# Optimization experiments

Hardware: AMD Instinct MI355X
Metric: run time of the kernel (lower is better)

The kernel has to match this reference:

```python
import jax, jax.numpy as jnp
import numpy as np

EMA_W = 0.99


def setup_inputs() -> dict:
    key = jax.random.key(0)
    k1, k2 = jax.random.split(key)
    B, C, H, W = 16, 8, 512, 512
    generated_masks = jax.random.normal(k1, (B, C, H, W), dtype=jnp.float32)
    prev_dist = jax.random.uniform(k2, (C,), dtype=jnp.float32)
    prev_dist = prev_dist / jnp.sum(prev_dist)  # a valid running distribution
    return {"generated_masks": generated_masks, "prev_dist": prev_dist}


def reference(generated_masks, prev_dist):
    # generated_masks: [B, C, H, W]; prev_dist: [C]
    B, C, H, W = generated_masks.shape
    num_classes = C
    norm_factor = 1.0 / num_classes

    # per-pixel argmax over channels -> [B, H, W]
    mask_classes = jnp.argmax(generated_masks, axis=1)

    # histogram over classes (fused equivalent of torch.unique + scatter)
    hist = jnp.zeros((num_classes,), dtype=jnp.float32).at[
        mask_classes.reshape(-1)
    ].add(1.0)

    total = B * H * W
    class_distribution = prev_dist * EMA_W + (1.0 - EMA_W) * hist / total

    balance = jnp.linalg.norm(
        (class_distribution - norm_factor) / (1.0 - norm_factor)
    )
    return balance, class_distribution
```

## Files before the change

kernel.cpp:

```cpp
#include <hip/hip_runtime.h>
#include <math.h>

#define HW        262144
#define HWQ       65536
#define CHW       2097152
#define NGROUPS   1048576
#define NBLOCKS   2048
#define NTHREADS  256
#define GSTRIDE   524288
#define TOTAL_PX  4194304.0f

__global__ __launch_bounds__(NTHREADS, 8)
void argmax_hist_kernel(const float* __restrict__ masks,
                        unsigned int* __restrict__ partial) {
    const int tid = threadIdx.x;
    int cnt[8] = {0, 0, 0, 0, 0, 0, 0, 0};

    const int gbase = blockIdx.x * NTHREADS + tid;

    #pragma unroll
    for (int it = 0; it < 2; ++it) {
        const int g   = gbase + it * GSTRIDE;
        const int b   = g >> 16;
        const int hw4 = (g & 65535) << 2;
        const float4* p = (const float4*)(masks + (size_t)b * CHW + hw4);

        float4 v0 = p[0];
        float4 v1 = p[1 * HWQ];
        float4 v2 = p[2 * HWQ];
        float4 v3 = p[3 * HWQ];
        float4 v4 = p[4 * HWQ];
        float4 v5 = p[5 * HWQ];
        float4 v6 = p[6 * HWQ];
        float4 v7 = p[7 * HWQ];

        float bv0 = v0.x, bv1 = v0.y, bv2 = v0.z, bv3 = v0.w;
        int   bi0 = 0,    bi1 = 0,    bi2 = 0,    bi3 = 0;

        #define STEP(vv, c)                                                   \
            bi0 = ((vv).x > bv0) ? (c) : bi0;  bv0 = ((vv).x > bv0) ? (vv).x : bv0; \
            bi1 = ((vv).y > bv1) ? (c) : bi1;  bv1 = ((vv).y > bv1) ? (vv).y : bv1; \
            bi2 = ((vv).z > bv2) ? (c) : bi2;  bv2 = ((vv).z > bv2) ? (vv).z : bv2; \
            bi3 = ((vv).w > bv3) ? (c) : bi3;  bv3 = ((vv).w > bv3) ? (vv).w : bv3;
        STEP(v1, 1) STEP(v2, 2) STEP(v3, 3) STEP(v4, 4)
        STEP(v5, 5) STEP(v6, 6) STEP(v7, 7)
        #undef STEP

        #pragma unroll
        for (int k = 0; k < 8; ++k) {
            cnt[k] += (bi0 == k) + (bi1 == k) + (bi2 == k) + (bi3 == k);
        }
    }

    #pragma unroll
    for (int k = 0; k < 8; ++k) {
        #pragma unroll
        for (int off = 32; off >= 1; off >>= 1) {
            cnt[k] += __shfl_down(cnt[k], off, 64);
        }
    }

    __shared__ int lds[32];
    const int lane = tid & 63;
    const int wid  = tid >> 6;
    if (lane == 0) {
        #pragma unroll
        for (int k = 0; k < 8; ++k) lds[wid * 8 + k] = cnt[k];
    }
    __syncthreads();
    if (tid < 8) {
        unsigned int s = (unsigned int)(lds[tid] + lds[8 + tid] + lds[16 + tid] + lds[24 + tid]);
        partial[blockIdx.x * 8 + tid] = s;
    }
}

__global__ __launch_bounds__(256)
void finalize_kernel(const unsigned int* __restrict__ partial,
                     const float* __restrict__ prev,
                     float* __restrict__ out) {
    __shared__ float s[256];
    const int t = threadIdx.x;
    const int c = t & 7;
    const int j = t >> 3;

    unsigned int sum = 0;
    for (int row = j; row < NBLOCKS; row += 32) {
        sum += partial[row * 8 + c];
    }
    s[t] = (float)sum;
    __syncthreads();

    if (t < 8) {
        float h = 0.0f;
        #pragma unroll
        for (int k = 0; k < 32; ++k) h += s[t + 8 * k];
        float dist = prev[t] * 0.99f + 0.01f * h / TOTAL_PX;
        out[1 + t] = dist;
        float d = (dist - 0.125f) / 0.875f;
        s[t] = d * d;
    }
    __syncthreads();
    if (t == 0) {
        float acc = 0.0f;
        #pragma unroll
        for (int k = 0; k < 8; ++k) acc += s[k];
        out[0] = sqrtf(acc);
    }
}

extern "C" void kernel_launch(void* const* d_in, const int* in_sizes, int n_in,
                              void* d_out, int out_size, void* d_ws, size_t ws_size,
                              hipStream_t stream) {
    const float* masks = (const float*)d_in[0];
    const float* prev  = (const float*)d_in[1];
    float* out = (float*)d_out;
    unsigned int* partial = (unsigned int*)d_ws;

    argmax_hist_kernel<<<NBLOCKS, NTHREADS, 0, stream>>>(masks, partial);
    finalize_kernel<<<1, 256, 0, stream>>>(partial, prev, out);
}
```

Before: 198.9 us.

## Use ballot-popcount histogram, nontemporal loads, one group per thread

Each thread now handles one pixel group instead of two, so the grid doubles to 4096 blocks. Loads become nontemporal vector loads, since the input is streamed once. The per-class shuffle-reduction tree is replaced with wavefront ballot plus popcount, which removes many shuffle instructions. The trade-off is less memory-level parallelism per thread, twice as many partial rows for the finalize kernel to sum, and more block-level sync and LDS overhead.

```diff
diff --git a/kernel.cpp b/kernel.cpp
--- a/kernel.cpp
+++ b/kernel.cpp
@@ -5,67 +5,50 @@
 #define HWQ       65536
 #define CHW       2097152
 #define NGROUPS   1048576
-#define NBLOCKS   2048
+#define NBLOCKS   4096
 #define NTHREADS  256
-#define GSTRIDE   524288
 #define TOTAL_PX  4194304.0f
+
+typedef float v4f __attribute__((ext_vector_type(4)));
 
 __global__ __launch_bounds__(NTHREADS, 8)
 void argmax_hist_kernel(const float* __restrict__ masks,
                         unsigned int* __restrict__ partial) {
     const int tid = threadIdx.x;
-    int cnt[8] = {0, 0, 0, 0, 0, 0, 0, 0};
+    const int g   = blockIdx.x * NTHREADS + tid;
+    const int b   = g >> 16;
+    const int hw4 = (g & 65535) << 2;
+    const v4f* p = (const v4f*)(masks + (size_t)b * CHW + hw4);
 
-    const int gbase = blockIdx.x * NTHREADS + tid;
+    v4f v0 = __builtin_nontemporal_load(p + 0 * HWQ);
+    v4f v1 = __builtin_nontemporal_load(p + 1 * HWQ);
+    v4f v2 = __builtin_nontemporal_load(p + 2 * HWQ);
+    v4f v3 = __builtin_nontemporal_load(p + 3 * HWQ);
+    v4f v4 = __builtin_nontemporal_load(p + 4 * HWQ);
+    v4f v5 = __builtin_nontemporal_load(p + 5 * HWQ);
+    v4f v6 = __builtin_nontemporal_load(p + 6 * HWQ);
+    v4f v7 = __builtin_nontemporal_load(p + 7 * HWQ);
 
-    #pragma unroll
-    for (int it = 0; it < 2; ++it) {
-        const int g   = gbase + it * GSTRIDE;
-        const int b   = g >> 16;
-        const int hw4 = (g & 65535) << 2;
-        const float4* p = (const float4*)(masks + (size_t)b * CHW + hw4);
+    float bv0 = v0.x, bv1 = v0.y, bv2 = v0.z, bv3 = v0.w;
+    int   bi0 = 0,    bi1 = 0,    bi2 = 0,    bi3 = 0;
 
-        float4 v0 = p[0];
-        float4 v1 = p[1 * HWQ];
-        float4 v2 = p[2 * HWQ];
-        float4 v3 = p[3 * HWQ];
-        float4 v4 = p[4 * HWQ];
-        float4 v5 = p[5 * HWQ];
-        float4 v6 = p[6 * HWQ];
-        float4 v7 = p[7 * HWQ];
+    #define STEP(vv, c)                                                         \
+        bi0 = ((vv).x > bv0) ? (c) : bi0;  bv0 = ((vv).x > bv0) ? (vv).x : bv0; \
+        bi1 = ((vv).y > bv1) ? (c) : bi1;  bv1 = ((vv).y > bv1) ? (vv).y : bv1; \
+        bi2 = ((vv).z > bv2) ? (c) : bi2;  bv2 = ((vv).z > bv2) ? (vv).z : bv2; \
+        bi3 = ((vv).w > bv3) ? (c) : bi3;  bv3 = ((vv).w > bv3) ? (vv).w : bv3;
+    STEP(v1, 1) STEP(v2, 2) STEP(v3, 3) STEP(v4, 4)
+    STEP(v5, 5) STEP(v6, 6) STEP(v7, 7)
+    #undef STEP
 
-        float bv0 = v0.x, bv1 = v0.y, bv2 = v0.z, bv3 = v0.w;
-        int   bi0 = 0,    bi1 = 0,    bi2 = 0,    bi3 = 0;
-
-        #define STEP(vv, c)                                                   \
-            bi0 = ((vv).x > bv0) ? (c) : bi0;  bv0 = ((vv).x > bv0) ? (vv).x : bv0; \
-            bi1 = ((vv).y > bv1) ? (c) : bi1;  bv1 = ((vv).y > bv1) ? (vv).y : bv1; \
-            bi2 = ((vv).z > bv2) ? (c) : bi2;  bv2 = ((vv).z > bv2) ? (vv).z : bv2; \
-            bi3 = ((vv).w > bv3) ? (c) : bi3;  bv3 = ((vv).w > bv3) ? (vv).w : bv3;
-        STEP(v1, 1) STEP(v2, 2) STEP(v3, 3) STEP(v4, 4)
-        STEP(v5, 5) STEP(v6, 6) STEP(v7, 7)
-        #undef STEP
-
-        #pragma unroll
-        for (int k = 0; k < 8; ++k) {
-            cnt[k] += (bi0 == k) + (bi1 == k) + (bi2 == k) + (bi3 == k);
-        }
-    }
-
+    const int lane = tid & 63;
+    const int wid  = tid >> 6;
+    __shared__ int lds[32];
     #pragma unroll
     for (int k = 0; k < 8; ++k) {
-        #pragma unroll
-        for (int off = 32; off >= 1; off >>= 1) {
-            cnt[k] += __shfl_down(cnt[k], off, 64);
-        }
-    }
-
-    __shared__ int lds[32];
-    const int lane = tid & 63;
-    const int wid  = tid >> 6;
-    if (lane == 0) {
-        #pragma unroll
-        for (int k = 0; k < 8; ++k) lds[wid * 8 + k] = cnt[k];
+        int c = __popcll(__ballot(bi0 == k)) + __popcll(__ballot(bi1 == k))
+              + __popcll(__ballot(bi2 == k)) + __popcll(__ballot(bi3 == k));
+        if (lane == 0) lds[wid * 8 + k] = c;
     }
     __syncthreads();
     if (tid < 8) {
```

Result: no change. 197.2 us (-0.9%).
